# Optimization experiments

Hardware: AMD Instinct MI355X
Metric: run time of the kernel (lower is better)

## Reference

```python
import jax, jax.numpy as jnp
import numpy as np

B, L, C = 2, 8192, 256
K, NLEV = 17, 4
HALF = K // 2


def setup_inputs() -> dict:
    key = jax.random.key(0)
    ks = jax.random.split(key, 10)
    s = 0.02
    return {
        "x": jax.random.normal(ks[0], (B, L, C), jnp.float32),
        "stem_w": jax.random.normal(ks[1], (C, C, 2), jnp.float32) * s,   # Conv1d (out,in,k)
        "stem_b": jax.random.normal(ks[2], (C,), jnp.float32) * s,
        "qkv_w": jax.random.normal(ks[3], (3 * C, C), jnp.float32) * s,
        "width_w": jax.random.normal(ks[4], (1, C), jnp.float32) * s,
        "width_b": jax.random.normal(ks[5], (1,), jnp.float32) * s,
        "out_w": jax.random.normal(ks[6], (C, C), jnp.float32) * s,
        "query": jax.random.normal(ks[7], (NLEV * C,), jnp.float32) * s,
        "film_w": jax.random.normal(ks[8], (2 * C, NLEV * C), jnp.float32) * s,
        "film_b": jax.random.normal(ks[9], (2 * C,), jnp.float32) * s,
    }


def _local_attn(h, qkv_w, width_w, width_b, out_w):
    # h: (b, l, c); 1D local windowed attention with learned sigmoid distance mask
    b, l, c = h.shape
    rel_dist = jnp.abs(jnp.arange(K, dtype=h.dtype) - HALF)  # (K,)
    max_dist = float(HALF)
    scale = c ** -0.5
    qkv = h @ qkv_w.T
    q, k, v = jnp.split(qkv, 3, axis=-1)
    width = jax.nn.sigmoid(h @ width_w.T + width_b) * max_dist + 0.5  # (b,l,1)
    k_pad = jnp.pad(k, ((0, 0), (HALF, HALF), (0, 0)))
    v_pad = jnp.pad(v, ((0, 0), (HALF, HALF), (0, 0)))
    idx = jnp.arange(l)[:, None] + jnp.arange(K)[None, :]  # (l,K) indices into padded seq
    k_win = k_pad[:, idx]  # (b,l,K,c)
    v_win = v_pad[:, idx]  # (b,l,K,c)
    scores = jnp.einsum('blc,blwc->blw', q, k_win) * scale
    soft_mask = jax.nn.sigmoid((width - rel_dist) * 5.0)  # (b,l,K)
    scores = scores - (1.0 - soft_mask) * 10000.0
    attn = jax.nn.softmax(scores, axis=-1)
    o = jnp.einsum('blw,blwc->blc', attn, v_win)
    return (o + v) @ out_w.T


def _forward(x, stem_w, stem_b, qkv_w, width_w, width_b, out_w, query, film_w, film_b):
    b, l, c = x.shape
    # stem conv: Conv1d(C, C, kernel=2, padding=1), then narrow to first l positions
    h = jnp.transpose(x, (0, 2, 1))  # (B,C,L)
    h = jax.lax.conv_general_dilated(h, stem_w, (1,), [(1, 1)],
                                     dimension_numbers=('NCH', 'OIH', 'NCH'))
    h = h[:, :, :l] + stem_b[None, :, None]
    h = jnp.transpose(h, (0, 2, 1))  # (B,L,C)
    levels = []
    for i in range(NLEV):
        h = _local_attn(h, qkv_w, width_w, width_b, out_w)
        levels.append(h)
        if i < NLEV - 1:  # avg_pool(kernel=2, stride=2)
            bl = h.shape[1]
            h = h.reshape(b, bl // 2, 2, c).mean(axis=2)
    # nearest upsample each coarser level back to L (factors are exact powers of 2)
    ups = [levels[0]]
    for lvl in levels[1:]:
        ups.append(jnp.repeat(lvl, l // lvl.shape[1], axis=1))
    concat = jnp.concatenate(ups, axis=-1)  # (B,L,NLEV*C)
    gattn = jax.nn.softmax(concat @ query, axis=-1)  # (B,L)
    global_ctx = jnp.einsum('bl,bld->bd', gattn, concat)  # (B,NLEV*C)
    film = global_ctx @ film_w.T + film_b  # (B,2C)
    scale_f, bias_f = jnp.split(film, 2, axis=-1)
    return levels[0] * (1.0 + scale_f[:, None, :]) + bias_f[:, None, :]


def reference(x, stem_w, stem_b, qkv_w, width_w, width_b, out_w, query, film_w, film_b):
    return _forward(x, stem_w, stem_b, qkv_w, width_w, width_b, out_w, query, film_w, film_b)
```

## Files before the change

kernel.cpp:

```cpp
#include <hip/hip_runtime.h>
#include <math.h>

#define L_SEQ 8192
#define B_SZ  2
#define CH    256
#define NLEV  4

typedef __attribute__((ext_vector_type(8))) short bf16x8;
typedef __attribute__((ext_vector_type(4))) float f32x4;

static __device__ __forceinline__ float sigmoidf_(float x) {
    return 1.0f / (1.0f + expf(-x));
}

static __device__ __forceinline__ float bf2f_(unsigned short u) {
    union { unsigned int ui; float f; } x;
    x.ui = ((unsigned int)u) << 16;
    return x.f;
}
static __device__ __forceinline__ unsigned short f2b_(float f) {
    union { float f; unsigned int u; } x;
    x.f = f;
    unsigned int lsb = (x.u >> 16) & 1u;
    unsigned int r = x.u + 0x7fffu + lsb;
    return (unsigned short)(r >> 16);
}
static __device__ __forceinline__ float4 ldb4_(const unsigned short* p) {
    ushort4 u = *(const ushort4*)p;
    return make_float4(bf2f_(u.x), bf2f_(u.y), bf2f_(u.z), bf2f_(u.w));
}

__global__ void prep_kernel(const float* __restrict__ x,
                            const float* __restrict__ qkv_w,
                            const float* __restrict__ out_w,
                            const float* __restrict__ stem_w,
                            unsigned short* __restrict__ x16g,
                            unsigned short* __restrict__ qw16,
                            unsigned short* __restrict__ ow16,
                            unsigned short* __restrict__ sw16)
{
    int i = blockIdx.x * 256 + threadIdx.x;
    if (i < 256) { x16g[i] = 0; return; }
    i -= 256;
    if (i < 4194304) { x16g[256 + i] = f2b_(x[i]); return; }
    i -= 4194304;
    if (i < 196608) { qw16[i] = f2b_(qkv_w[i]); return; }
    i -= 196608;
    if (i < 65536) { ow16[i] = f2b_(out_w[i]); return; }
    i -= 65536;
    {
        int k = i & 511, n = i >> 9;
        float v = (k < 256) ? stem_w[(size_t)n * 512 + k * 2]
                            : stem_w[(size_t)n * 512 + (k - 256) * 2 + 1];
        sw16[i] = f2b_(v);
    }
}

__global__ __launch_bounds__(256) void stem_gemm_bf16(
    const unsigned short* __restrict__ x16g, const unsigned short* __restrict__ W,
    unsigned short* __restrict__ outB, const float* __restrict__ bias)
{
    __shared__ unsigned short As[128 * 32];
    __shared__ unsigned short Bs[128 * 32];
    const int tid  = threadIdx.x;
    const int wave = tid >> 6;
    const int lane = tid & 63;
    const int bm = blockIdx.y * 128;
    const int bn = blockIdx.x * 128;
    const int wm = (wave & 1) * 64;
    const int wn = (wave >> 1) * 64;
    const int srow = lane >> 2;
    const int scol = (lane & 3) * 8;

    f32x4 acc[4][4] = {};

    for (int k0 = 0; k0 < 512; k0 += 32) {
        __syncthreads();
        #pragma unroll
        for (int c = 0; c < 2; ++c) {
            const int chunk = c * 4 + wave;
            const int row = bm + chunk * 16 + srow;
            const int t = row & (L_SEQ - 1);
            const unsigned short* ga;
            if (k0 < 256)
                ga = x16g + (t > 0 ? (size_t)row * 256 : 0) + k0 + scol;
            else
                ga = x16g + ((size_t)row + 1) * 256 + (k0 - 256) + scol;
            const unsigned short* gw = W + (size_t)(bn + chunk * 16 + srow) * 512 + k0 + scol;
            __builtin_amdgcn_global_load_lds(
                (const __attribute__((address_space(1))) void*)ga,
                (__attribute__((address_space(3))) void*)(As + chunk * 16 * 32),
                16, 0, 0);
            __builtin_amdgcn_global_load_lds(
                (const __attribute__((address_space(1))) void*)gw,
                (__attribute__((address_space(3))) void*)(Bs + chunk * 16 * 32),
                16, 0, 0);
        }
        __syncthreads();

        bf16x8 af[4], bf[4];
        const int fr = lane & 15;
        const int kk = (lane >> 4) * 8;
        #pragma unroll
        for (int i = 0; i < 4; ++i) {
            af[i] = *(const bf16x8*)(As + (wm + i * 16 + fr) * 32 + kk);
            bf[i] = *(const bf16x8*)(Bs + (wn + i * 16 + fr) * 32 + kk);
        }
        #pragma unroll
        for (int i = 0; i < 4; ++i)
            #pragma unroll
            for (int j = 0; j < 4; ++j)
                acc[i][j] = __builtin_amdgcn_mfma_f32_16x16x32_bf16(
                    af[i], bf[j], acc[i][j], 0, 0, 0);
    }

    const int cn = lane & 15;
    const int cr = (lane >> 4) * 4;
    #pragma unroll
    for (int i = 0; i < 4; ++i)
        #pragma unroll
        for (int r = 0; r < 4; ++r) {
            const int m = bm + wm + i * 16 + cr + r;
            #pragma unroll
            for (int j = 0; j < 4; ++j) {
                const int n = bn + wn + j * 16 + cn;
                outB[(size_t)m * CH + n] = f2b_(acc[i][j][r] + bias[n]);
            }
        }
}

__global__ __launch_bounds__(256) void gemm_bf16(
    const unsigned short* __restrict__ A, const unsigned short* __restrict__ W,
    unsigned short* __restrict__ outB, int M, int N, int Kd)
{
    __shared__ unsigned short As[128 * 32];
    __shared__ unsigned short Bs[128 * 32];
    const int tid  = threadIdx.x;
    const int wave = tid >> 6;
    const int lane = tid & 63;
    const int bm = blockIdx.y * 128;
    const int bn = blockIdx.x * 128;
    const int wm = (wave & 1) * 64;
    const int wn = (wave >> 1) * 64;
    const int srow = lane >> 2;
    const int scol = (lane & 3) * 8;

    f32x4 acc[4][4] = {};

    for (int k0 = 0; k0 < Kd; k0 += 32) {
        __syncthreads();
        #pragma unroll
        for (int c = 0; c < 2; ++c) {
            const int chunk = c * 4 + wave;
            const int row = chunk * 16 + srow;
            const unsigned short* ga = A + (size_t)(bm + row) * Kd + k0 + scol;
            const unsigned short* gw = W + (size_t)(bn + row) * Kd + k0 + scol;
            __builtin_amdgcn_global_load_lds(
                (const __attribute__((address_space(1))) void*)ga,
                (__attribute__((address_space(3))) void*)(As + chunk * 16 * 32),
                16, 0, 0);
            __builtin_amdgcn_global_load_lds(
                (const __attribute__((address_space(1))) void*)gw,
                (__attribute__((address_space(3))) void*)(Bs + chunk * 16 * 32),
                16, 0, 0);
        }
        __syncthreads();

        bf16x8 af[4], bf[4];
        const int fr = lane & 15;
        const int kk = (lane >> 4) * 8;
        #pragma unroll
        for (int i = 0; i < 4; ++i) {
            af[i] = *(const bf16x8*)(As + (wm + i * 16 + fr) * 32 + kk);
            bf[i] = *(const bf16x8*)(Bs + (wn + i * 16 + fr) * 32 + kk);
        }
        #pragma unroll
        for (int i = 0; i < 4; ++i)
            #pragma unroll
            for (int j = 0; j < 4; ++j)
                acc[i][j] = __builtin_amdgcn_mfma_f32_16x16x32_bf16(
                    af[i], bf[j], acc[i][j], 0, 0, 0);
    }

    const int cn = lane & 15;
    const int cr = (lane >> 4) * 4;
    #pragma unroll
    for (int i = 0; i < 4; ++i)
        #pragma unroll
        for (int r = 0; r < 4; ++r) {
            const int m = bm + wm + i * 16 + cr + r;
            const size_t rowoff = (size_t)m * N;
            #pragma unroll
            for (int j = 0; j < 4; ++j)
                outB[rowoff + bn + wn + j * 16 + cn] = f2b_(acc[i][j][r]);
        }
}

__global__ __launch_bounds__(256) void attn_fused_kernel(
    const unsigned short* __restrict__ qkv, const unsigned short* __restrict__ h16,
    const float* __restrict__ ww, const float* __restrict__ wbp,
    const unsigned short* __restrict__ ow,
    unsigned short* __restrict__ l16o, unsigned short* __restrict__ dsB, int l)
{
    __shared__ unsigned short kv[22528];
    __shared__ unsigned short pb[4 * 512];

    const int tid  = threadIdx.x;
    const int wave = tid >> 6;
    const int lane = tid & 63;
    const int q    = lane >> 4;
    const int n    = lane & 15;

    const int blocks_per_seq = l >> 6;
    const int b  = blockIdx.x / blocks_per_seq;
    const int t0 = (blockIdx.x % blocks_per_seq) << 6;
    const size_t seqbase = (size_t)b * l;
    const int row0 = t0 + wave * 16;

    #pragma unroll
    for (int i = 0; i < 10; ++i) {
        int task = i * 256 + tid;
        int r = task >> 5, chunk = task & 31;
        int grow = t0 - 8 + r;
        bf16x8 val = {0, 0, 0, 0, 0, 0, 0, 0};
        if (grow >= 0 && grow < l)
            val = *(const bf16x8*)(qkv + (seqbase + grow) * 768 + 256 + chunk * 8);
        *(bf16x8*)(kv + r * 272 + chunk * 8) = val;
    }

    float wdot = 0.0f;
    {
        const unsigned short* hrow = h16 + (seqbase + row0 + n) * 256 + q * 64;
        #pragma unroll
        for (int jj = 0; jj < 8; ++jj) {
            bf16x8 hv = *(const bf16x8*)(hrow + jj * 8);
            float4 wa = *((const float4*)(ww + q * 64 + jj * 8));
            float4 wc = *((const float4*)(ww + q * 64 + jj * 8 + 4));
            wdot += bf2f_(((unsigned short*)&hv)[0]) * wa.x
                  + bf2f_(((unsigned short*)&hv)[1]) * wa.y
                  + bf2f_(((unsigned short*)&hv)[2]) * wa.z
                  + bf2f_(((unsigned short*)&hv)[3]) * wa.w
                  + bf2f_(((unsigned short*)&hv)[4]) * wc.x
                  + bf2f_(((unsigned short*)&hv)[5]) * wc.y
                  + bf2f_(((unsigned short*)&hv)[6]) * wc.z
                  + bf2f_(((unsigned short*)&hv)[7]) * wc.w;
        }
    }
    wdot += __shfl_xor(wdot, 16, 64);
    wdot += __shfl_xor(wdot, 32, 64);
    const float w_n = sigmoidf_(wdot + wbp[0]) * 8.0f + 0.5f;

    __syncthreads();

    bf16x8 qf[8];
    const unsigned short* qrow = qkv + (seqbase + row0 + n) * 768;
    #pragma unroll
    for (int kk = 0; kk < 8; ++kk)
        qf[kk] = *(const bf16x8*)(qrow + kk * 32 + q * 8);

    f32x4 accS[2] = {};
    __builtin_amdgcn_s_setprio(1);
    #pragma unroll
    for (int kk = 0; kk < 8; ++kk) {
        #pragma unroll
        for (int h = 0; h < 2; ++h) {
            bf16x8 bk = *(const bf16x8*)(kv + (wave * 16 + h * 16 + n) * 272 +
                                         kk * 32 + q * 8);
            accS[h] = __builtin_amdgcn_mfma_f32_16x16x32_bf16(
                qf[kk], bk, accS[h], 0, 0, 0);
        }
    }
    __builtin_amdgcn_s_setprio(0);

    float wd[4];
    #pragma unroll
    for (int r = 0; r < 4; ++r) wd[r] = __shfl(w_n, q * 4 + r, 64);

    float s[2][4];
    #pragma unroll
    for (int h = 0; h < 2; ++h)
        #pragma unroll
        for (int r = 0; r < 4; ++r) {
            int ii = q * 4 + r;
            int c  = h * 16 + n;
            int w  = c - ii;
            float dist = fabsf((float)w - 8.0f);
            float sm = sigmoidf_((wd[r] - dist) * 5.0f);
            float v = accS[h][r] * 0.0625f - (1.0f - sm) * 10000.0f;
            s[h][r] = (w >= 0 && w <= 16) ? v : -3.0e38f;
        }

    float mx[4], sum[4];
    #pragma unroll
    for (int r = 0; r < 4; ++r) mx[r] = fmaxf(s[0][r], s[1][r]);
    #pragma unroll
    for (int m = 1; m < 16; m <<= 1)
        #pragma unroll
        for (int r = 0; r < 4; ++r) mx[r] = fmaxf(mx[r], __shfl_xor(mx[r], m, 64));
    float e[2][4];
    #pragma unroll
    for (int h = 0; h < 2; ++h)
        #pragma unroll
        for (int r = 0; r < 4; ++r) e[h][r] = expf(s[h][r] - mx[r]);
    #pragma unroll
    for (int r = 0; r < 4; ++r) sum[r] = e[0][r] + e[1][r];
    #pragma unroll
    for (int m = 1; m < 16; m <<= 1)
        #pragma unroll
        for (int r = 0; r < 4; ++r) sum[r] += __shfl_xor(sum[r], m, 64);

    #pragma unroll
    for (int h = 0; h < 2; ++h)
        #pragma unroll
        for (int r = 0; r < 4; ++r) {
            int ii = q * 4 + r, c = h * 16 + n;
            float p = e[h][r] / sum[r];
            if (c == ii + 8) p += 1.0f;
            pb[wave * 512 + ii * 32 + c] = f2b_(p);
        }
    __syncthreads();

    #pragma unroll
    for (int p5 = 0; p5 < 5; ++p5)
        #pragma unroll
        for (int cc = 0; cc < 2; ++cc) {
            int r = p5 * 16 + (tid & 15);
            int chunk = cc * 16 + (tid >> 4);
            int grow = t0 - 8 + r;
            bf16x8 val = {0, 0, 0, 0, 0, 0, 0, 0};
            if (grow >= 0 && grow < l)
                val = *(const bf16x8*)(qkv + (seqbase + grow) * 768 + 512 + chunk * 8);
            #pragma unroll
            for (int jj = 0; jj < 8; ++jj)
                kv[(chunk * 8 + jj) * 88 + r] = ((unsigned short*)&val)[jj];
        }
    __syncthreads();

    bf16x8 pf = *(const bf16x8*)(pb + wave * 512 + n * 32 + q * 8);
    f32x4 po[8];
    __builtin_amdgcn_s_setprio(1);
    #pragma unroll
    for (int c = 0; c < 8; ++c) {
        bf16x8 vf = *(const bf16x8*)(kv + (c * 16 + n) * 88 + wave * 16 + q * 8);
        f32x4 z = {};
        po[c] = __builtin_amdgcn_mfma_f32_16x16x32_bf16(pf, vf, z, 0, 0, 0);
    }
    __builtin_amdgcn_s_setprio(0);
    __syncthreads();
    {
        char* orsB = (char*)kv;
        #pragma unroll
        for (int c = 0; c < 8; ++c)
            #pragma unroll
            for (int r = 0; r < 4; ++r) {
                const int row = wave * 16 + q * 4 + r;
                *(unsigned short*)(orsB +
                    ((row * 256 + c * 32 + 2 * n) ^ ((row & 7) << 4))) = f2b_(po[c][r]);
            }
    }
    __builtin_amdgcn_s_setprio(1);
    #pragma unroll
    for (int c = 0; c < 8; ++c) {
        bf16x8 vf = *(const bf16x8*)(kv + ((c + 8) * 16 + n) * 88 + wave * 16 + q * 8);
        f32x4 z = {};
        po[c] = __builtin_amdgcn_mfma_f32_16x16x32_bf16(pf, vf, z, 0, 0, 0);
    }
    __builtin_amdgcn_s_setprio(0);
    __syncthreads();
    {
        char* orsB = (char*)(kv + 8192);
        #pragma unroll
        for (int c = 0; c < 8; ++c)
            #pragma unroll
            for (int r = 0; r < 4; ++r) {
                const int row = wave * 16 + q * 4 + r;
                *(unsigned short*)(orsB +
                    ((row * 256 + c * 32 + 2 * n) ^ ((row & 7) << 4))) = f2b_(po[c][r]);
            }
    }
    __syncthreads();

    f32x4 acc[4][4] = {};
    const unsigned short* owb = ow + (size_t)(wave * 64) * 256;
    #pragma unroll
    for (int k0 = 0; k0 < 256; k0 += 32) {
        const char* Ab = (const char*)(kv + ((k0 & 128) ? 8192 : 0));
        const int kb = ((k0 & 127) + q * 8) * 2;
        bf16x8 af[4], bv[4];
        #pragma unroll
        for (int i = 0; i < 4; ++i) {
            const int row = i * 16 + n;
            af[i] = *(const bf16x8*)(Ab + ((row * 256 + kb) ^ ((n & 7) << 4)));
        }
        #pragma unroll
        for (int j = 0; j < 4; ++j)
            bv[j] = *(const bf16x8*)(owb + (size_t)(j * 16 + n) * 256 + k0 + q * 8);
        __builtin_amdgcn_s_setprio(1);
        #pragma unroll
        for (int i = 0; i < 4; ++i)
            #pragma unroll
            for (int j = 0; j < 4; ++j)
                acc[i][j] = __builtin_amdgcn_mfma_f32_16x16x32_bf16(
                    af[i], bv[j], acc[i][j], 0, 0, 0);
        __builtin_amdgcn_s_setprio(0);
    }

    const size_t gbase = seqbase + t0;
    #pragma unroll
    for (int i = 0; i < 4; ++i) {
        const int rl = i * 16 + q * 4;
        #pragma unroll
        for (int j = 0; j < 4; ++j) {
            const int col = wave * 64 + j * 16 + n;
            float v0 = acc[i][j][0], v1 = acc[i][j][1];
            float v2 = acc[i][j][2], v3 = acc[i][j][3];
            size_t r0 = (gbase + rl) * CH + col;
            l16o[r0]           = f2b_(v0);
            l16o[r0 + CH]      = f2b_(v1);
            l16o[r0 + 2 * CH]  = f2b_(v2);
            l16o[r0 + 3 * CH]  = f2b_(v3);
            if (dsB) {
                size_t d0 = ((gbase + rl) >> 1) * CH + col;
                dsB[d0]      = f2b_(0.5f * (v0 + v1));
                dsB[d0 + CH] = f2b_(0.5f * (v2 + v3));
            }
        }
    }
}

__global__ __launch_bounds__(1024) void tail_ctx_kernel(
    const unsigned short* __restrict__ l0, const unsigned short* __restrict__ l1,
    const unsigned short* __restrict__ l2, const unsigned short* __restrict__ l3,
    const float* __restrict__ query, float* __restrict__ partials,
    float* __restrict__ denomP)
{
    __shared__ float eS[128];
    const int tid = threadIdx.x;
    const int chunk = blockIdx.x, b = blockIdx.y;
    const int t0 = chunk * 128;
    const unsigned short* levp[4] = {l0, l1, l2, l3};

    const int w = tid >> 6, lane = tid & 63;
    const int lev = lane >> 4, c0 = (lane & 15) * 16;
    const unsigned short* lpbase = levp[lev] + (size_t)b * (L_SEQ >> lev) * CH;
    const float* qp = query + lev * CH + c0;
    float4 q0 = *(const float4*)(qp);
    float4 q1 = *(const float4*)(qp + 4);
    float4 q2 = *(const float4*)(qp + 8);
    float4 q3 = *(const float4*)(qp + 12);
    #pragma unroll
    for (int j = 0; j < 8; ++j) {
        int t = t0 + w * 8 + j;
        const unsigned short* p = lpbase + (size_t)(t >> lev) * CH + c0;
        float4 h0 = ldb4_(p), h1 = ldb4_(p + 4), h2 = ldb4_(p + 8), h3 = ldb4_(p + 12);
        float part = h0.x * q0.x + h0.y * q0.y + h0.z * q0.z + h0.w * q0.w
                   + h1.x * q1.x + h1.y * q1.y + h1.z * q1.z + h1.w * q1.w
                   + h2.x * q2.x + h2.y * q2.y + h2.z * q2.z + h2.w * q2.w
                   + h3.x * q3.x + h3.y * q3.y + h3.z * q3.z + h3.w * q3.w;
        #pragma unroll
        for (int m = 1; m < 64; m <<= 1) part += __shfl_xor(part, m, 64);
        if (lane == 0) eS[w * 8 + j] = expf(part);
    }
    __syncthreads();

    if (tid == 0) {
        float ds = 0.0f;
        #pragma unroll 8
        for (int i = 0; i < 128; ++i) ds += eS[i];
        denomP[b * 64 + chunk] = ds;
    }

    const int dlev = tid >> 8, c = tid & 255;
    const unsigned short* lp = levp[dlev] + (size_t)b * (L_SEQ >> dlev) * CH;
    float acc = 0.0f;
    #pragma unroll 4
    for (int t = t0; t < t0 + 128; ++t)
        acc += eS[t - t0] * bf2f_(lp[(size_t)(t >> dlev) * CH + c]);
    partials[(size_t)(b * 64 + chunk) * 1024 + tid] = acc;
}

__global__ __launch_bounds__(256) void ctx_reduce_kernel(
    const float* __restrict__ partials, const float* __restrict__ denomP,
    float* __restrict__ ctx)
{
    const int b = blockIdx.y;
    const int d = blockIdx.x * 256 + threadIdx.x;
    float acc = 0.0f;
    #pragma unroll
    for (int c = 0; c < 64; ++c) acc += partials[(size_t)(b * 64 + c) * 1024 + d];
    float den = 0.0f;
    #pragma unroll
    for (int c = 0; c < 64; ++c) den += denomP[b * 64 + c];
    ctx[b * 1024 + d] = acc / den;
}

__global__ __launch_bounds__(256) void film_kernel(
    const float* __restrict__ ctx, const float* __restrict__ fw,
    const float* __restrict__ fb, float* __restrict__ film)
{
    const int lane = threadIdx.x & 63;
    const int j = blockIdx.x * 4 + (threadIdx.x >> 6);
    float acc0 = 0.0f, acc1 = 0.0f;
    #pragma unroll
    for (int r = 0; r < 4; ++r) {
        float4 w4 = *((const float4*)(fw + (size_t)j * 1024 + r * 256) + lane);
        float4 c0 = *((const float4*)(ctx + r * 256) + lane);
        float4 c1 = *((const float4*)(ctx + 1024 + r * 256) + lane);
        acc0 += w4.x * c0.x + w4.y * c0.y + w4.z * c0.z + w4.w * c0.w;
        acc1 += w4.x * c1.x + w4.y * c1.y + w4.z * c1.z + w4.w * c1.w;
    }
    #pragma unroll
    for (int m = 1; m < 64; m <<= 1) {
        acc0 += __shfl_xor(acc0, m, 64);
        acc1 += __shfl_xor(acc1, m, 64);
    }
    if (lane == 0) {
        float b = fb[j];
        film[j] = acc0 + b;
        film[512 + j] = acc1 + b;
    }
}

__global__ void final_kernel(const unsigned short* __restrict__ lev0,
                             const float* __restrict__ film,
                             float* __restrict__ out)
{
    size_t n4 = ((size_t)blockIdx.x * 256 + threadIdx.x) * 4;
    int c = (int)(n4 & (CH - 1));
    int b = (int)(n4 >> 21);
    float4 h = ldb4_(lev0 + n4);
    const float* fs = film + b * 512;
    float4 o;
    o.x = h.x * (1.0f + fs[c + 0]) + fs[256 + c + 0];
    o.y = h.y * (1.0f + fs[c + 1]) + fs[256 + c + 1];
    o.z = h.z * (1.0f + fs[c + 2]) + fs[256 + c + 2];
    o.w = h.w * (1.0f + fs[c + 3]) + fs[256 + c + 3];
    *(float4*)(out + n4) = o;
}

extern "C" void kernel_launch(void* const* d_in, const int* in_sizes, int n_in,
                              void* d_out, int out_size, void* d_ws, size_t ws_size,
                              hipStream_t stream) {
    const float* x       = (const float*)d_in[0];
    const float* stem_w  = (const float*)d_in[1];
    const float* stem_b  = (const float*)d_in[2];
    const float* qkv_w   = (const float*)d_in[3];
    const float* width_w = (const float*)d_in[4];
    const float* width_b = (const float*)d_in[5];
    const float* out_w   = (const float*)d_in[6];
    const float* query   = (const float*)d_in[7];
    const float* film_w  = (const float*)d_in[8];
    const float* film_b  = (const float*)d_in[9];
    float* out = (float*)d_out;
    float* ws  = (float*)d_ws;

    float* partials = ws;
    float* denomP   = partials + 131072;
    float* ctx      = denomP + 128;
    float* film     = ctx + 2048;
    unsigned short* x16g  = (unsigned short*)(film + 1024);
    unsigned short* h16_0 = x16g + 4194560;
    unsigned short* h16_1 = h16_0 + 4194304;
    unsigned short* h16_2 = h16_1 + 2097152;
    unsigned short* h16_3 = h16_2 + 1048576;
    unsigned short* qkv16 = h16_3 + 524288;
    unsigned short* ov16  = qkv16 + 12582912;
    unsigned short* l16_0 = ov16 + 4194304;
    unsigned short* l16_1 = l16_0 + 4194304;
    unsigned short* l16_2 = l16_1 + 2097152;
    unsigned short* l16_3 = l16_2 + 1048576;
    unsigned short* qw16  = l16_3 + 524288;
    unsigned short* ow16  = qw16 + 196608;
    unsigned short* sw16  = ow16 + 65536;
    unsigned short* h16[4]  = {h16_0, h16_1, h16_2, h16_3};
    unsigned short* l16[4]  = {l16_0, l16_1, l16_2, l16_3};
    (void)ov16;

    prep_kernel<<<(256 + 4194304 + 196608 + 65536 + 131072) / 256, 256, 0, stream>>>(
        x, qkv_w, out_w, stem_w, x16g, qw16, ow16, sw16);

    stem_gemm_bf16<<<dim3(CH / 128, B_SZ * L_SEQ / 128), 256, 0, stream>>>(
        x16g, sw16, h16_0, stem_b);

    for (int i = 0; i < NLEV; ++i) {
        const int l = L_SEQ >> i;
        const int M = B_SZ * l;
        gemm_bf16<<<dim3(768 / 128, M / 128), 256, 0, stream>>>(
            h16[i], qw16, qkv16, M, 768, CH);
        attn_fused_kernel<<<M / 64, 256, 0, stream>>>(
            qkv16, h16[i], width_w, width_b, ow16,
            l16[i], (i < NLEV - 1) ? h16[i + 1] : nullptr, l);
    }

    tail_ctx_kernel<<<dim3(64, B_SZ), 1024, 0, stream>>>(
        l16_0, l16_1, l16_2, l16_3, query, partials, denomP);
    ctx_reduce_kernel<<<dim3(4, B_SZ), 256, 0, stream>>>(partials, denomP, ctx);
    film_kernel<<<128, 256, 0, stream>>>(ctx, film_w, film_b, film);
    final_kernel<<<(B_SZ * L_SEQ * CH) / 1024, 256, 0, stream>>>(l16_0, film, out);
}
```

Measured before the change: 257.9 us.

## Rewrite fused local attention as single-wave blocks with XCD-aware block remapping

The 256-thread, 64-row fused attention kernel is replaced by a one-wave block that handles 16 rows. K fragments now come straight from global memory, and V is prefetched into registers and then transposed into LDS, so every __syncthreads is gone. Block ids are remapped so that neighbouring tiles land on the same XCD, which should improve L2 reuse of the overlapping K/V halos. In exchange, each 16-row tile reloads its halo (32 rows instead of 80 rows per 64), and every block streams the full out_w matrix from global or L2 memory.

```diff
diff --git a/kernel.cpp b/kernel.cpp
--- a/kernel.cpp
+++ b/kernel.cpp
@@ -196,41 +196,46 @@
         }
 }
 
-__global__ __launch_bounds__(256) void attn_fused_kernel(
+__global__ __launch_bounds__(64) void attn_fused_w1(
     const unsigned short* __restrict__ qkv, const unsigned short* __restrict__ h16,
     const float* __restrict__ ww, const float* __restrict__ wbp,
     const unsigned short* __restrict__ ow,
     unsigned short* __restrict__ l16o, unsigned short* __restrict__ dsB, int l)
 {
-    __shared__ unsigned short kv[22528];
-    __shared__ unsigned short pb[4 * 512];
-
-    const int tid  = threadIdx.x;
-    const int wave = tid >> 6;
-    const int lane = tid & 63;
-    const int q    = lane >> 4;
-    const int n    = lane & 15;
-
-    const int blocks_per_seq = l >> 6;
-    const int b  = blockIdx.x / blocks_per_seq;
-    const int t0 = (blockIdx.x % blocks_per_seq) << 6;
-    const size_t seqbase = (size_t)b * l;
-    const int row0 = t0 + wave * 16;
-
-    #pragma unroll
-    for (int i = 0; i < 10; ++i) {
-        int task = i * 256 + tid;
-        int r = task >> 5, chunk = task & 31;
-        int grow = t0 - 8 + r;
-        bf16x8 val = {0, 0, 0, 0, 0, 0, 0, 0};
-        if (grow >= 0 && grow < l)
-            val = *(const bf16x8*)(qkv + (seqbase + grow) * 768 + 256 + chunk * 8);
-        *(bf16x8*)(kv + r * 272 + chunk * 8) = val;
+    __shared__ __align__(16) unsigned short vt[256 * 40];
+    __shared__ __align__(16) unsigned short pb[16 * 32];
+    __shared__ __align__(16) unsigned short ors[16 * 256];
+
+    const int lane = threadIdx.x;
+    const int q = lane >> 4;
+    const int n = lane & 15;
+
+    int bid = blockIdx.x;
+    const int cpx = gridDim.x >> 3;
+    bid = (bid & 7) * cpx + (bid >> 3);
+
+    const int bps = l >> 4;
+    const int b  = bid / bps;
+    const int t0 = (bid % bps) << 4;
+    const long long seqbase = (long long)b * l;
+
+    bf16x8 vv[16];
+    {
+        const int r = lane & 31;
+        const int grow = t0 - 8 + r;
+        const bool vok = (grow >= 0 && grow < l);
+        const unsigned short* vbase = qkv + (seqbase + grow) * 768 + 512 + (lane >> 5) * 8;
+        #pragma unroll
+        for (int i = 0; i < 16; ++i) {
+            bf16x8 val = {0, 0, 0, 0, 0, 0, 0, 0};
+            if (vok) val = *(const bf16x8*)(vbase + i * 16);
+            vv[i] = val;
+        }
     }
 
     float wdot = 0.0f;
     {
-        const unsigned short* hrow = h16 + (seqbase + row0 + n) * 256 + q * 64;
+        const unsigned short* hrow = h16 + (seqbase + t0 + n) * 256 + q * 64;
         #pragma unroll
         for (int jj = 0; jj < 8; ++jj) {
             bf16x8 hv = *(const bf16x8*)(hrow + jj * 8);
@@ -250,27 +255,37 @@
     wdot += __shfl_xor(wdot, 32, 64);
     const float w_n = sigmoidf_(wdot + wbp[0]) * 8.0f + 0.5f;
 
-    __syncthreads();
-
     bf16x8 qf[8];
-    const unsigned short* qrow = qkv + (seqbase + row0 + n) * 768;
+    const unsigned short* qrow = qkv + (seqbase + t0 + n) * 768;
     #pragma unroll
     for (int kk = 0; kk < 8; ++kk)
         qf[kk] = *(const bf16x8*)(qrow + kk * 32 + q * 8);
 
     f32x4 accS[2] = {};
-    __builtin_amdgcn_s_setprio(1);
-    #pragma unroll
-    for (int kk = 0; kk < 8; ++kk) {
-        #pragma unroll
-        for (int h = 0; h < 2; ++h) {
-            bf16x8 bk = *(const bf16x8*)(kv + (wave * 16 + h * 16 + n) * 272 +
-                                         kk * 32 + q * 8);
+    #pragma unroll
+    for (int h = 0; h < 2; ++h) {
+        const int grow = t0 - 8 + h * 16 + n;
+        const bool ok = (grow >= 0 && grow < l);
+        const unsigned short* kb = qkv + (seqbase + grow) * 768 + 256 + q * 8;
+        #pragma unroll
+        for (int kk = 0; kk < 8; ++kk) {
+            bf16x8 bk = {0, 0, 0, 0, 0, 0, 0, 0};
+            if (ok) bk = *(const bf16x8*)(kb + kk * 32);
             accS[h] = __builtin_amdgcn_mfma_f32_16x16x32_bf16(
                 qf[kk], bk, accS[h], 0, 0, 0);
         }
     }
-    __builtin_amdgcn_s_setprio(0);
+
+    {
+        const int r = lane & 31;
+        #pragma unroll
+        for (int i = 0; i < 16; ++i) {
+            const int chunk = 2 * i + (lane >> 5);
+            #pragma unroll
+            for (int jj = 0; jj < 8; ++jj)
+                vt[(chunk * 8 + jj) * 40 + r] = ((unsigned short*)&vv[i])[jj];
+        }
+    }
 
     float wd[4];
     #pragma unroll
@@ -316,114 +331,52 @@
             int ii = q * 4 + r, c = h * 16 + n;
             float p = e[h][r] / sum[r];
             if (c == ii + 8) p += 1.0f;
-            pb[wave * 512 + ii * 32 + c] = f2b_(p);
-        }
-    __syncthreads();
-
-    #pragma unroll
-    for (int p5 = 0; p5 < 5; ++p5)
-        #pragma unroll
-        for (int cc = 0; cc < 2; ++cc) {
-            int r = p5 * 16 + (tid & 15);
-            int chunk = cc * 16 + (tid >> 4);
-            int grow = t0 - 8 + r;
-            bf16x8 val = {0, 0, 0, 0, 0, 0, 0, 0};
-            if (grow >= 0 && grow < l)
-                val = *(const bf16x8*)(qkv + (seqbase + grow) * 768 + 512 + chunk * 8);
-            #pragma unroll
-            for (int jj = 0; jj < 8; ++jj)
-                kv[(chunk * 8 + jj) * 88 + r] = ((unsigned short*)&val)[jj];
-        }
-    __syncthreads();
-
-    bf16x8 pf = *(const bf16x8*)(pb + wave * 512 + n * 32 + q * 8);
-    f32x4 po[8];
-    __builtin_amdgcn_s_setprio(1);
-    #pragma unroll
-    for (int c = 0; c < 8; ++c) {
-        bf16x8 vf = *(const bf16x8*)(kv + (c * 16 + n) * 88 + wave * 16 + q * 8);
+            pb[ii * 32 + c] = f2b_(p);
+        }
+
+    bf16x8 pf = *(const bf16x8*)(pb + n * 32 + q * 8);
+    char* orsB = (char*)ors;
+    #pragma unroll
+    for (int ct = 0; ct < 16; ++ct) {
+        bf16x8 vf = *(const bf16x8*)(vt + (ct * 16 + n) * 40 + q * 8);
         f32x4 z = {};
-        po[c] = __builtin_amdgcn_mfma_f32_16x16x32_bf16(pf, vf, z, 0, 0, 0);
-    }
-    __builtin_amdgcn_s_setprio(0);
-    __syncthreads();
-    {
-        char* orsB = (char*)kv;
-        #pragma unroll
-        for (int c = 0; c < 8; ++c)
-            #pragma unroll
-            for (int r = 0; r < 4; ++r) {
-                const int row = wave * 16 + q * 4 + r;
-                *(unsigned short*)(orsB +
-                    ((row * 256 + c * 32 + 2 * n) ^ ((row & 7) << 4))) = f2b_(po[c][r]);
-            }
-    }
-    __builtin_amdgcn_s_setprio(1);
-    #pragma unroll
-    for (int c = 0; c < 8; ++c) {
-        bf16x8 vf = *(const bf16x8*)(kv + ((c + 8) * 16 + n) * 88 + wave * 16 + q * 8);
-        f32x4 z = {};
-        po[c] = __builtin_amdgcn_mfma_f32_16x16x32_bf16(pf, vf, z, 0, 0, 0);
-    }
-    __builtin_amdgcn_s_setprio(0);
-    __syncthreads();
-    {
-        char* orsB = (char*)(kv + 8192);
-        #pragma unroll
-        for (int c = 0; c < 8; ++c)
-            #pragma unroll
-            for (int r = 0; r < 4; ++r) {
-                const int row = wave * 16 + q * 4 + r;
-                *(unsigned short*)(orsB +
-                    ((row * 256 + c * 32 + 2 * n) ^ ((row & 7) << 4))) = f2b_(po[c][r]);
-            }
-    }
-    __syncthreads();
-
-    f32x4 acc[4][4] = {};
-    const unsigned short* owb = ow + (size_t)(wave * 64) * 256;
+        f32x4 o = __builtin_amdgcn_mfma_f32_16x16x32_bf16(pf, vf, z, 0, 0, 0);
+        #pragma unroll
+        for (int r = 0; r < 4; ++r) {
+            const int row = q * 4 + r;
+            *(unsigned short*)(orsB +
+                ((row * 512 + (ct * 16 + n) * 2) ^ ((row & 7) << 4))) = f2b_(o[r]);
+        }
+    }
+
+    f32x4 acc[16] = {};
     #pragma unroll
     for (int k0 = 0; k0 < 256; k0 += 32) {
-        const char* Ab = (const char*)(kv + ((k0 & 128) ? 8192 : 0));
-        const int kb = ((k0 & 127) + q * 8) * 2;
-        bf16x8 af[4], bv[4];
-        #pragma unroll
-        for (int i = 0; i < 4; ++i) {
-            const int row = i * 16 + n;
-            af[i] = *(const bf16x8*)(Ab + ((row * 256 + kb) ^ ((n & 7) << 4)));
-        }
-        #pragma unroll
-        for (int j = 0; j < 4; ++j)
-            bv[j] = *(const bf16x8*)(owb + (size_t)(j * 16 + n) * 256 + k0 + q * 8);
-        __builtin_amdgcn_s_setprio(1);
-        #pragma unroll
-        for (int i = 0; i < 4; ++i)
-            #pragma unroll
-            for (int j = 0; j < 4; ++j)
-                acc[i][j] = __builtin_amdgcn_mfma_f32_16x16x32_bf16(
-                    af[i], bv[j], acc[i][j], 0, 0, 0);
-        __builtin_amdgcn_s_setprio(0);
-    }
-
-    const size_t gbase = seqbase + t0;
-    #pragma unroll
-    for (int i = 0; i < 4; ++i) {
-        const int rl = i * 16 + q * 4;
-        #pragma unroll
-        for (int j = 0; j < 4; ++j) {
-            const int col = wave * 64 + j * 16 + n;
-            float v0 = acc[i][j][0], v1 = acc[i][j][1];
-            float v2 = acc[i][j][2], v3 = acc[i][j][3];
-            size_t r0 = (gbase + rl) * CH + col;
-            l16o[r0]           = f2b_(v0);
-            l16o[r0 + CH]      = f2b_(v1);
-            l16o[r0 + 2 * CH]  = f2b_(v2);
-            l16o[r0 + 3 * CH]  = f2b_(v3);
-            if (dsB) {
-                size_t d0 = ((gbase + rl) >> 1) * CH + col;
-                dsB[d0]      = f2b_(0.5f * (v0 + v1));
-                dsB[d0 + CH] = f2b_(0.5f * (v2 + v3));
-            }
+        bf16x8 af = *(const bf16x8*)(orsB +
+            ((n * 512 + (k0 + q * 8) * 2) ^ ((n & 7) << 4)));
+        #pragma unroll
+        for (int j = 0; j < 16; ++j) {
+            bf16x8 bv = *(const bf16x8*)(ow + (size_t)(j * 16 + n) * 256 + k0 + q * 8);
+            acc[j] = __builtin_amdgcn_mfma_f32_16x16x32_bf16(af, bv, acc[j], 0, 0, 0);
+        }
+    }
+
+    const long long gbase = seqbase + t0;
+    const int rl = q * 4;
+    #pragma unroll
+    for (int j = 0; j < 16; ++j) {
+        const int col = j * 16 + n;
+        float v0 = acc[j][0], v1 = acc[j][1];
+        float v2 = acc[j][2], v3 = acc[j][3];
+        size_t r0 = (size_t)(gbase + rl) * CH + col;
+        l16o[r0]          = f2b_(v0);
+        l16o[r0 + CH]     = f2b_(v1);
+        l16o[r0 + 2 * CH] = f2b_(v2);
+        l16o[r0 + 3 * CH] = f2b_(v3);
+        if (dsB) {
+            size_t d0 = (size_t)((gbase + rl) >> 1) * CH + col;
+            dsB[d0]      = f2b_(0.5f * (v0 + v1));
+            dsB[d0 + CH] = f2b_(0.5f * (v2 + v3));
         }
     }
 }
@@ -587,7 +540,7 @@
         const int M = B_SZ * l;
         gemm_bf16<<<dim3(768 / 128, M / 128), 256, 0, stream>>>(
             h16[i], qw16, qkv16, M, 768, CH);
-        attn_fused_kernel<<<M / 64, 256, 0, stream>>>(
+        attn_fused_w1<<<M / 16, 64, 0, stream>>>(
             qkv16, h16[i], width_w, width_b, ow16,
             l16[i], (i < NLEV - 1) ? h16[i + 1] : nullptr, l);
     }
```

New measurement: 274.4 us. 1.06x slower.
